# Performance work log

Hardware: AMD Instinct MI355X
Metric: run time of the kernel (lower is better)

The kernel has to match this reference:

```python
import jax, jax.numpy as jnp
import numpy as np

RADIUS = 1.0
NSAMPLE = 1024  # num_votes
EPS = 1e-5     # BatchNorm eps


def _bn2(x, gamma, beta):
    # BatchNorm over [B, C, NS]: stats per channel across (batch, sample)
    m = jnp.mean(x, axis=(0, 2), keepdims=True)
    v = jnp.var(x, axis=(0, 2), keepdims=True)
    return gamma[None, :, None] * (x - m) * jax.lax.rsqrt(v + EPS) + beta[None, :, None]


def _bn1(x, gamma, beta):
    # BatchNorm over [B, C] (conv1d head with length 1): stats across batch
    m = jnp.mean(x, axis=0, keepdims=True)
    v = jnp.var(x, axis=0, keepdims=True)
    return gamma[None, :] * (x - m) * jax.lax.rsqrt(v + EPS) + beta[None, :]


def setup_inputs() -> dict:
    key = jax.random.key(0)
    ks = jax.random.split(key, 16)
    B, N, C = 8, 65536, 256
    def w(k, o, i):
        return jax.random.normal(k, (o, i), jnp.float32) * (1.0 / np.sqrt(i))
    inp = {
        'xyz': jax.random.normal(ks[0], (B, N, 3), jnp.float32),
        'features': jax.random.normal(ks[1], (B, C, N), jnp.float32),
        # shared MLP (conv2d 1x1 + BN + ReLU) x3, input channels = C+3 (use_xyz)
        'w1': w(ks[2], 128, C + 3), 'b1': jnp.zeros(128), 'g1': jnp.ones(128), 'be1': jnp.zeros(128),
        'w2': w(ks[3], 128, 128),   'b2': jnp.zeros(128), 'g2': jnp.ones(128), 'be2': jnp.zeros(128),
        'w3': w(ks[4], 128, 128),   'b3': jnp.zeros(128), 'g3': jnp.ones(128), 'be3': jnp.zeros(128),
        # conv1d head
        'hw1': w(ks[5], 128, 128), 'hb1': jnp.zeros(128), 'hg1': jnp.ones(128), 'hbe1': jnp.zeros(128),
        'hw2': w(ks[6], 128, 128), 'hb2': jnp.zeros(128), 'hg2': jnp.ones(128), 'hbe2': jnp.zeros(128),
        'hw3': w(ks[7], 12, 128),  'hb3': jnp.zeros(12),
    }
    return inp


def reference(xyz, features, w1, b1, g1, be1, w2, b2, g2, be2, w3, b3, g3, be3,
              hw1, hb1, hg1, hbe1, hw2, hb2, hg2, hbe2, hw3, hb3):
    B, N, _ = xyz.shape
    # FPS with npoint=1 deterministically selects point 0
    center = xyz[:, 0, :]                                   # [B,3]
    d2 = jnp.sum((xyz - center[:, None, :]) ** 2, axis=-1)   # [B,N]
    mask = d2 < RADIUS * RADIUS
    ar = jnp.arange(N)
    # ball query: first NSAMPLE in-radius indices (index order), pad with first hit
    order = jnp.argsort(jnp.where(mask, ar, N + ar), axis=1)[:, :NSAMPLE]  # [B,NS]
    valid = jnp.take_along_axis(mask, order, axis=1)
    inds = jnp.where(valid, order, order[:, :1])              # [B,NS]
    g_xyz = (jnp.take_along_axis(xyz, inds[:, :, None], axis=1) - center[:, None, :]) / RADIUS  # [B,NS,3]
    g_feat = jax.vmap(lambda f, i: f[:, i])(features, inds)    # [B,C,NS]
    g = jnp.concatenate([jnp.swapaxes(g_xyz, 1, 2), g_feat], axis=1)  # [B,C+3,NS]

    def mlp(x, w, b, gm, bt):
        y = jnp.einsum('oc,bcn->bon', w, x) + b[None, :, None]
        return jax.nn.relu(_bn2(y, gm, bt))

    h = mlp(g, w1, b1, g1, be1)
    h = mlp(h, w2, b2, g2, be2)
    h = mlp(h, w3, b3, g3, be3)
    f = jnp.max(h, axis=2)                                    # [B,128] maxpool over nsample

    net = jax.nn.relu(_bn1(f @ hw1.T + hb1, hg1, hbe1))
    net = jax.nn.relu(_bn1(net @ hw2.T + hb2, hg2, hbe2))
    net = net @ hw3.T + hb3                                   # [B,12]

    center_out = center + net[:, 0:3]
    size = net[:, 3:6]
    rot_6d = net[:, 6:12]
    return (center_out, size, rot_6d)
```

## Files before the change

kernel.cpp:

```cpp
#include <hip/hip_runtime.h>
#include <hip/hip_bf16.h>
#include <stdint.h>

#define BATCH 8
#define NPTS  65536
#define CFEAT 256
#define K1    259
#define K1PAD 288
#define CH    128
#define NS    1024
#define EPSF  1e-5f
#define INVN  (1.0f / (BATCH * NS))

__device__ __forceinline__ unsigned fenc(float f) {
  unsigned u = __float_as_uint(f);
  return (u & 0x80000000u) ? ~u : (u | 0x80000000u);
}
__device__ __forceinline__ float fdec(unsigned k) {
  unsigned u = (k & 0x80000000u) ? (k & 0x7fffffffu) : ~k;
  return __uint_as_float(u);
}

__global__ __launch_bounds__(1024) void k_select(const float* __restrict__ xyz,
                                                 int* __restrict__ inds,
                                                 float* __restrict__ center,
                                                 float* __restrict__ sums,
                                                 unsigned* __restrict__ maxk,
                                                 unsigned* __restrict__ mink) {
  int b = blockIdx.x;
  int tid = threadIdx.x;
  int lane = tid & 63, wid = tid >> 6;

  if (b == 0) {
    if (tid < 3 * 2 * CH) sums[tid] = 0.f;
    if (tid < BATCH * CH) { maxk[tid] = 0u; mink[tid] = 0xFFFFFFFFu; }
  }

  const float* xb = xyz + (size_t)b * NPTS * 3;
  float cx = xb[0], cy = xb[1], cz = xb[2];
  if (tid < 3) center[b * 3 + tid] = xb[tid];

  __shared__ int wcnt[16];
  int total = 0;
  int* ib = inds + b * NS;

  for (int base = 0; base < NPTS; base += 1024) {
    int i = base + tid;
    float dx = xb[(size_t)i * 3 + 0] - cx;
    float dy = xb[(size_t)i * 3 + 1] - cy;
    float dz = xb[(size_t)i * 3 + 2] - cz;
    float d2 = dx * dx + dy * dy + dz * dz;
    bool pred = d2 < 1.0f;
    unsigned long long bal = __ballot(pred);
    if (lane == 0) wcnt[wid] = (int)__popcll(bal);
    __syncthreads();
    int woff = 0, itot = 0;
#pragma unroll
    for (int w = 0; w < 16; ++w) {
      int c = wcnt[w];
      if (w < wid) woff += c;
      itot += c;
    }
    int pos = total + woff + (int)__popcll(bal & ((1ull << lane) - 1ull));
    if (pred && pos < NS) ib[pos] = i;
    total += itot;
    __syncthreads();
    if (total >= NS) break;
  }
  for (int j = total + tid; j < NS; j += 1024) ib[j] = 0;
}

__device__ __forceinline__ void store_and_stats(float* __restrict__ yb,
                                                float* __restrict__ sums,
                                                const float* __restrict__ bias,
                                                float acc[4][4],
                                                int n0, int tx, int ty) {
#pragma unroll
  for (int r = 0; r < 4; ++r) {
    int o = ty * 4 + r;
    float bs = bias[o];
    float4 v = make_float4(acc[r][0] + bs, acc[r][1] + bs,
                           acc[r][2] + bs, acc[r][3] + bs);
    *(float4*)&yb[(size_t)o * NS + n0 + tx * 4] = v;
    float s = v.x + v.y + v.z + v.w;
    float q = v.x * v.x + v.y * v.y + v.z * v.z + v.w * v.w;
    s += __shfl_xor(s, 1, 64); q += __shfl_xor(q, 1, 64);
    s += __shfl_xor(s, 2, 64); q += __shfl_xor(q, 2, 64);
    s += __shfl_xor(s, 4, 64); q += __shfl_xor(q, 4, 64);
    if (tx == 0) {
      atomicAdd(&sums[o], s);
      atomicAdd(&sums[CH + o], q);
    }
  }
}

__global__ __launch_bounds__(256) void k_gemm1(const float* __restrict__ xyz,
                                               const float* __restrict__ feat,
                                               const int* __restrict__ inds,
                                               const float* __restrict__ center,
                                               const float* __restrict__ W,
                                               const float* __restrict__ bias,
                                               float* __restrict__ y,
                                               float* __restrict__ sums) {
  __shared__ float Ws[32][132];
  __shared__ float Xs[K1PAD][36];
  __shared__ int   ids[32];
  __shared__ float cenl[3];
  int b = blockIdx.y;
  int n0 = blockIdx.x * 32;
  int tid = threadIdx.x;
  if (tid < 32) ids[tid] = inds[b * NS + n0 + tid];
  if (tid < 3)  cenl[tid] = center[b * 3 + tid];
  __syncthreads();

  const float* featb = feat + (size_t)b * CFEAT * NPTS;
  const float* xyzb  = xyz + (size_t)b * NPTS * 3;

  if (tid < 96) {
    int k = tid >> 5, j = tid & 31;
    Xs[k][j] = xyzb[(size_t)ids[j] * 3 + k] - cenl[k];
  }
#pragma unroll 8
  for (int e = tid; e < CFEAT * 32; e += 256) {
    int k = e >> 5, j = e & 31;
    Xs[3 + k][j] = featb[(size_t)k * NPTS + ids[j]];
  }
#pragma unroll
  for (int e = tid; e < 29 * 32; e += 256) {
    Xs[K1 + (e >> 5)][e & 31] = 0.f;
  }

  int tx = tid & 7, ty = tid >> 3;
  float acc[4][4];
#pragma unroll
  for (int r = 0; r < 4; ++r)
#pragma unroll
    for (int j = 0; j < 4; ++j) acc[r][j] = 0.f;

  for (int k0 = 0; k0 < K1PAD; k0 += 32) {
#pragma unroll
    for (int i = 0; i < 16; ++i) {
      int e = tid + 256 * i;
      int o = e >> 5, kk = e & 31;
      int k = k0 + kk;
      Ws[kk][o] = (k < K1) ? W[o * K1 + k] : 0.f;
    }
    __syncthreads();
#pragma unroll
    for (int kk = 0; kk < 32; ++kk) {
      float4 xv = *(const float4*)&Xs[k0 + kk][tx * 4];
      float4 wv = *(const float4*)&Ws[kk][ty * 4];
      acc[0][0] += wv.x * xv.x; acc[0][1] += wv.x * xv.y; acc[0][2] += wv.x * xv.z; acc[0][3] += wv.x * xv.w;
      acc[1][0] += wv.y * xv.x; acc[1][1] += wv.y * xv.y; acc[1][2] += wv.y * xv.z; acc[1][3] += wv.y * xv.w;
      acc[2][0] += wv.z * xv.x; acc[2][1] += wv.z * xv.y; acc[2][2] += wv.z * xv.z; acc[2][3] += wv.z * xv.w;
      acc[3][0] += wv.w * xv.x; acc[3][1] += wv.w * xv.y; acc[3][2] += wv.w * xv.z; acc[3][3] += wv.w * xv.w;
    }
    __syncthreads();
  }
  store_and_stats(y + (size_t)b * CH * NS, sums, bias, acc, n0, tx, ty);
}

template <bool LAST>
__global__ __launch_bounds__(256) void k_gemm23(const float* __restrict__ x,
                                                const float* __restrict__ sums_prev,
                                                const float* __restrict__ gamma,
                                                const float* __restrict__ beta,
                                                const float* __restrict__ W,
                                                const float* __restrict__ bias,
                                                float* __restrict__ y,
                                                float* __restrict__ sums_out,
                                                unsigned* __restrict__ maxk,
                                                unsigned* __restrict__ mink) {
  __shared__ float Ws[32][132];
  __shared__ float Xs[CH][36];
  __shared__ float scl[CH], shf[CH];
  int b = blockIdx.y;
  int n0 = blockIdx.x * 32;
  int tid = threadIdx.x;
  if (tid < CH) {
    float s = sums_prev[tid], q = sums_prev[CH + tid];
    float mean = s * INVN;
    float var = fmaxf(q * INVN - mean * mean, 0.f);
    float sc = gamma[tid] * rsqrtf(var + EPSF);
    scl[tid] = sc;
    shf[tid] = beta[tid] - mean * sc;
  }
  __syncthreads();

  const float* xb = x + (size_t)b * CH * NS;
#pragma unroll
  for (int e = tid; e < CH * 32; e += 256) {
    int k = e >> 5, j = e & 31;
    float v = xb[(size_t)k * NS + n0 + j];
    Xs[k][j] = fmaxf(scl[k] * v + shf[k], 0.f);
  }

  int tx = tid & 7, ty = tid >> 3;
  float acc[4][4];
#pragma unroll
  for (int r = 0; r < 4; ++r)
#pragma unroll
    for (int j = 0; j < 4; ++j) acc[r][j] = 0.f;

  for (int k0 = 0; k0 < CH; k0 += 32) {
#pragma unroll
    for (int i = 0; i < 16; ++i) {
      int e = tid + 256 * i;
      int o = e >> 5, kk = e & 31;
      Ws[kk][o] = W[o * CH + k0 + kk];
    }
    __syncthreads();
#pragma unroll
    for (int kk = 0; kk < 32; ++kk) {
      float4 xv = *(const float4*)&Xs[k0 + kk][tx * 4];
      float4 wv = *(const float4*)&Ws[kk][ty * 4];
      acc[0][0] += wv.x * xv.x; acc[0][1] += wv.x * xv.y; acc[0][2] += wv.x * xv.z; acc[0][3] += wv.x * xv.w;
      acc[1][0] += wv.y * xv.x; acc[1][1] += wv.y * xv.y; acc[1][2] += wv.y * xv.z; acc[1][3] += wv.y * xv.w;
      acc[2][0] += wv.z * xv.x; acc[2][1] += wv.z * xv.y; acc[2][2] += wv.z * xv.z; acc[2][3] += wv.z * xv.w;
      acc[3][0] += wv.w * xv.x; acc[3][1] += wv.w * xv.y; acc[3][2] += wv.w * xv.z; acc[3][3] += wv.w * xv.w;
    }
    __syncthreads();
  }

  if (!LAST) {
    store_and_stats(y + (size_t)b * CH * NS, sums_out, bias, acc, n0, tx, ty);
  } else {
#pragma unroll
    for (int r = 0; r < 4; ++r) {
      int o = ty * 4 + r;
      float bs = bias[o];
      float4 v = make_float4(acc[r][0] + bs, acc[r][1] + bs,
                             acc[r][2] + bs, acc[r][3] + bs);
      float s = v.x + v.y + v.z + v.w;
      float q = v.x * v.x + v.y * v.y + v.z * v.z + v.w * v.w;
      float mx = fmaxf(fmaxf(v.x, v.y), fmaxf(v.z, v.w));
      float mn = fminf(fminf(v.x, v.y), fminf(v.z, v.w));
      s += __shfl_xor(s, 1, 64); q += __shfl_xor(q, 1, 64);
      mx = fmaxf(mx, __shfl_xor(mx, 1, 64)); mn = fminf(mn, __shfl_xor(mn, 1, 64));
      s += __shfl_xor(s, 2, 64); q += __shfl_xor(q, 2, 64);
      mx = fmaxf(mx, __shfl_xor(mx, 2, 64)); mn = fminf(mn, __shfl_xor(mn, 2, 64));
      s += __shfl_xor(s, 4, 64); q += __shfl_xor(q, 4, 64);
      mx = fmaxf(mx, __shfl_xor(mx, 4, 64)); mn = fminf(mn, __shfl_xor(mn, 4, 64));
      if (tx == 0) {
        atomicAdd(&sums_out[o], s);
        atomicAdd(&sums_out[CH + o], q);
        atomicMax(&maxk[b * CH + o], fenc(mx));
        atomicMin(&mink[b * CH + o], fenc(mn));
      }
    }
  }
}

__global__ __launch_bounds__(128) void k_head(const float* __restrict__ sums3,
                                              const float* __restrict__ ga3, const float* __restrict__ be3,
                                              const unsigned* __restrict__ maxk, const unsigned* __restrict__ mink,
                                              const float* __restrict__ hw1, const float* __restrict__ hb1,
                                              const float* __restrict__ hg1, const float* __restrict__ hbe1,
                                              const float* __restrict__ hw2, const float* __restrict__ hb2,
                                              const float* __restrict__ hg2, const float* __restrict__ hbe2,
                                              const float* __restrict__ hw3, const float* __restrict__ hb3,
                                              const float* __restrict__ center,
                                              float* __restrict__ out) {
  __shared__ float A[BATCH * 128];
  __shared__ float Bm[BATCH * 128];
  int c = threadIdx.x;
  {
    float s = sums3[c], q = sums3[CH + c];
    float mean = s * INVN;
    float var = fmaxf(q * INVN - mean * mean, 0.f);
    float sc = ga3[c] * rsqrtf(var + EPSF);
    float sh = be3[c] - mean * sc;
#pragma unroll
    for (int b = 0; b < BATCH; ++b) {
      float ymax = fdec(maxk[b * CH + c]);
      float ymin = fdec(mink[b * CH + c]);
      float ye = (sc >= 0.f) ? ymax : ymin;
      A[b * 128 + c] = fmaxf(sc * ye + sh, 0.f);
    }
  }
  __syncthreads();

  {
    float v[BATCH];
    float bs = hb1[c];
#pragma unroll
    for (int b = 0; b < BATCH; ++b) v[b] = bs;
    const float4* w4 = (const float4*)hw1 + c * 32;
    for (int k4 = 0; k4 < 32; ++k4) {
      float4 w = w4[k4];
#pragma unroll
      for (int b = 0; b < BATCH; ++b) {
        const float* Ar = &A[b * 128 + k4 * 4];
        v[b] += Ar[0] * w.x + Ar[1] * w.y + Ar[2] * w.z + Ar[3] * w.w;
      }
    }
    float m = 0.f;
#pragma unroll
    for (int b = 0; b < BATCH; ++b) m += v[b];
    m *= (1.f / BATCH);
    float var = 0.f;
#pragma unroll
    for (int b = 0; b < BATCH; ++b) { float d = v[b] - m; var += d * d; }
    var *= (1.f / BATCH);
    float r = rsqrtf(var + EPSF);
    float ga = hg1[c], be = hbe1[c];
#pragma unroll
    for (int b = 0; b < BATCH; ++b)
      Bm[b * 128 + c] = fmaxf(ga * (v[b] - m) * r + be, 0.f);
  }
  __syncthreads();

  {
    float v[BATCH];
    float bs = hb2[c];
#pragma unroll
    for (int b = 0; b < BATCH; ++b) v[b] = bs;
    const float4* w4 = (const float4*)hw2 + c * 32;
    for (int k4 = 0; k4 < 32; ++k4) {
      float4 w = w4[k4];
#pragma unroll
      for (int b = 0; b < BATCH; ++b) {
        const float* Br = &Bm[b * 128 + k4 * 4];
        v[b] += Br[0] * w.x + Br[1] * w.y + Br[2] * w.z + Br[3] * w.w;
      }
    }
    float m = 0.f;
#pragma unroll
    for (int b = 0; b < BATCH; ++b) m += v[b];
    m *= (1.f / BATCH);
    float var = 0.f;
#pragma unroll
    for (int b = 0; b < BATCH; ++b) { float d = v[b] - m; var += d * d; }
    var *= (1.f / BATCH);
    float r = rsqrtf(var + EPSF);
    float ga = hg2[c], be = hbe2[c];
#pragma unroll
    for (int b = 0; b < BATCH; ++b)
      A[b * 128 + c] = fmaxf(ga * (v[b] - m) * r + be, 0.f);
  }
  __syncthreads();

  if (c < 96) {
    int b = c / 12, j = c % 12;
    float o = hb3[j];
    const float4* w4 = (const float4*)hw3 + j * 32;
    for (int k4 = 0; k4 < 32; ++k4) {
      float4 w = w4[k4];
      const float* Ar = &A[b * 128 + k4 * 4];
      o += Ar[0] * w.x + Ar[1] * w.y + Ar[2] * w.z + Ar[3] * w.w;
    }
    if (j < 3)      out[b * 3 + j] = center[b * 3 + j] + o;
    else if (j < 6) out[24 + b * 3 + (j - 3)] = o;
    else            out[48 + b * 6 + (j - 6)] = o;
  }
}

extern "C" void kernel_launch(void* const* d_in, const int* in_sizes, int n_in,
                              void* d_out, int out_size, void* d_ws, size_t ws_size,
                              hipStream_t stream) {
  const float* xyz  = (const float*)d_in[0];
  const float* feat = (const float*)d_in[1];
  const float* w1   = (const float*)d_in[2];
  const float* b1   = (const float*)d_in[3];
  const float* ga1  = (const float*)d_in[4];
  const float* be1  = (const float*)d_in[5];
  const float* w2   = (const float*)d_in[6];
  const float* b2   = (const float*)d_in[7];
  const float* ga2  = (const float*)d_in[8];
  const float* be2  = (const float*)d_in[9];
  const float* w3   = (const float*)d_in[10];
  const float* b3   = (const float*)d_in[11];
  const float* ga3  = (const float*)d_in[12];
  const float* be3  = (const float*)d_in[13];
  const float* hw1  = (const float*)d_in[14];
  const float* hb1  = (const float*)d_in[15];
  const float* hg1  = (const float*)d_in[16];
  const float* hbe1 = (const float*)d_in[17];
  const float* hw2  = (const float*)d_in[18];
  const float* hb2  = (const float*)d_in[19];
  const float* hg2  = (const float*)d_in[20];
  const float* hbe2 = (const float*)d_in[21];
  const float* hw3  = (const float*)d_in[22];
  const float* hb3  = (const float*)d_in[23];
  float* out = (float*)d_out;

  char* ws = (char*)d_ws;
  size_t off = 0;
  auto alloc = [&](size_t bytes) -> void* {
    void* p = ws + off;
    off = (off + bytes + 255) & ~(size_t)255;
    return p;
  };
  float*    sums1 = (float*)alloc(2 * CH * 4);
  float*    sums2 = (float*)alloc(2 * CH * 4);
  float*    sums3 = (float*)alloc(2 * CH * 4);
  unsigned* maxk  = (unsigned*)alloc((size_t)BATCH * CH * 4);
  unsigned* mink  = (unsigned*)alloc((size_t)BATCH * CH * 4);
  int*      inds  = (int*)alloc((size_t)BATCH * NS * 4);
  float*    center= (float*)alloc(BATCH * 3 * 4);
  float*    y1    = (float*)alloc((size_t)BATCH * CH * NS * 4);
  float*    y2    = (float*)alloc((size_t)BATCH * CH * NS * 4);

  k_select<<<dim3(BATCH), dim3(1024), 0, stream>>>(xyz, inds, center,
                                                   sums1, maxk, mink);
  k_gemm1<<<dim3(NS / 32, BATCH), dim3(256), 0, stream>>>(xyz, feat, inds, center,
                                                          w1, b1, y1, sums1);
  k_gemm23<false><<<dim3(NS / 32, BATCH), dim3(256), 0, stream>>>(y1, sums1, ga1, be1,
                                                                  w2, b2, y2, sums2,
                                                                  nullptr, nullptr);
  k_gemm23<true><<<dim3(NS / 32, BATCH), dim3(256), 0, stream>>>(y2, sums2, ga2, be2,
                                                                 w3, b3, nullptr, sums3,
                                                                 maxk, mink);
  k_head<<<dim3(1), dim3(128), 0, stream>>>(sums3, ga3, be3, maxk, mink,
                                            hw1, hb1, hg1, hbe1,
                                            hw2, hb2, hg2, hbe2, hw3, hb3,
                                            center, out);
}
```

Measured before the change: 851.4 us.

## Fuse whole pipeline into one cooperative persistent kernel with grid barriers

```diff
diff --git a/kernel.cpp b/kernel.cpp
--- a/kernel.cpp
+++ b/kernel.cpp
@@ -1,5 +1,4 @@
 #include <hip/hip_runtime.h>
-#include <hip/hip_bf16.h>
 #include <stdint.h>
 
 #define BATCH 8
@@ -11,6 +10,8 @@
 #define NS    1024
 #define EPSF  1e-5f
 #define INVN  (1.0f / (BATCH * NS))
+#define WS_STRIDE 132
+#define XS_STRIDE 36
 
 __device__ __forceinline__ unsigned fenc(float f) {
   unsigned u = __float_as_uint(f);
@@ -21,116 +22,199 @@
   return __uint_as_float(u);
 }
 
-__global__ __launch_bounds__(1024) void k_select(const float* __restrict__ xyz,
-                                                 int* __restrict__ inds,
-                                                 float* __restrict__ center,
-                                                 float* __restrict__ sums,
-                                                 unsigned* __restrict__ maxk,
-                                                 unsigned* __restrict__ mink) {
-  int b = blockIdx.x;
-  int tid = threadIdx.x;
-  int lane = tid & 63, wid = tid >> 6;
-
-  if (b == 0) {
-    if (tid < 3 * 2 * CH) sums[tid] = 0.f;
-    if (tid < BATCH * CH) { maxk[tid] = 0u; mink[tid] = 0xFFFFFFFFu; }
-  }
-
-  const float* xb = xyz + (size_t)b * NPTS * 3;
-  float cx = xb[0], cy = xb[1], cz = xb[2];
-  if (tid < 3) center[b * 3 + tid] = xb[tid];
-
-  __shared__ int wcnt[16];
-  int total = 0;
-  int* ib = inds + b * NS;
-
-  for (int base = 0; base < NPTS; base += 1024) {
-    int i = base + tid;
-    float dx = xb[(size_t)i * 3 + 0] - cx;
-    float dy = xb[(size_t)i * 3 + 1] - cy;
-    float dz = xb[(size_t)i * 3 + 2] - cz;
-    float d2 = dx * dx + dy * dy + dz * dz;
-    bool pred = d2 < 1.0f;
-    unsigned long long bal = __ballot(pred);
-    if (lane == 0) wcnt[wid] = (int)__popcll(bal);
-    __syncthreads();
-    int woff = 0, itot = 0;
-#pragma unroll
-    for (int w = 0; w < 16; ++w) {
-      int c = wcnt[w];
-      if (w < wid) woff += c;
-      itot += c;
-    }
-    int pos = total + woff + (int)__popcll(bal & ((1ull << lane) - 1ull));
-    if (pred && pos < NS) ib[pos] = i;
-    total += itot;
-    __syncthreads();
-    if (total >= NS) break;
-  }
-  for (int j = total + tid; j < NS; j += 1024) ib[j] = 0;
-}
-
-__device__ __forceinline__ void store_and_stats(float* __restrict__ yb,
-                                                float* __restrict__ sums,
-                                                const float* __restrict__ bias,
-                                                float acc[4][4],
-                                                int n0, int tx, int ty) {
+__device__ __forceinline__ float aload_f(const float* p) {
+  return __hip_atomic_load(p, __ATOMIC_RELAXED, __HIP_MEMORY_SCOPE_AGENT);
+}
+__device__ __forceinline__ void astore_f(float* p, float v) {
+  __hip_atomic_store(p, v, __ATOMIC_RELAXED, __HIP_MEMORY_SCOPE_AGENT);
+}
+__device__ __forceinline__ int aload_i(const int* p) {
+  return __hip_atomic_load(p, __ATOMIC_RELAXED, __HIP_MEMORY_SCOPE_AGENT);
+}
+__device__ __forceinline__ void astore_i(int* p, int v) {
+  __hip_atomic_store(p, v, __ATOMIC_RELAXED, __HIP_MEMORY_SCOPE_AGENT);
+}
+__device__ __forceinline__ unsigned aload_u(const unsigned* p) {
+  return __hip_atomic_load(p, __ATOMIC_RELAXED, __HIP_MEMORY_SCOPE_AGENT);
+}
+__device__ __forceinline__ void astore_u(unsigned* p, unsigned v) {
+  __hip_atomic_store(p, v, __ATOMIC_RELAXED, __HIP_MEMORY_SCOPE_AGENT);
+}
+
+__device__ __forceinline__ void gsync(unsigned* bar, unsigned target) {
+  __syncthreads();
+  if (threadIdx.x == 0) {
+    __hip_atomic_fetch_add(bar, 1u, __ATOMIC_ACQ_REL, __HIP_MEMORY_SCOPE_AGENT);
+    while (__hip_atomic_load(bar, __ATOMIC_ACQUIRE, __HIP_MEMORY_SCOPE_AGENT) < target)
+      __builtin_amdgcn_s_sleep(2);
+  }
+  __syncthreads();
+}
+
+#define FMA16(wv, xv) do { \
+  acc[0][0] += wv.x*xv.x; acc[0][1] += wv.x*xv.y; acc[0][2] += wv.x*xv.z; acc[0][3] += wv.x*xv.w; \
+  acc[1][0] += wv.y*xv.x; acc[1][1] += wv.y*xv.y; acc[1][2] += wv.y*xv.z; acc[1][3] += wv.y*xv.w; \
+  acc[2][0] += wv.z*xv.x; acc[2][1] += wv.z*xv.y; acc[2][2] += wv.z*xv.z; acc[2][3] += wv.z*xv.w; \
+  acc[3][0] += wv.w*xv.x; acc[3][1] += wv.w*xv.y; acc[3][2] += wv.w*xv.z; acc[3][3] += wv.w*xv.w; \
+} while (0)
+
+struct KParams {
+  const float *xyz, *feat;
+  const float *w1, *b1, *ga1, *be1;
+  const float *w2, *b2, *ga2, *be2;
+  const float *w3, *b3, *ga3, *be3;
+  const float *hw1, *hb1, *hg1, *hbe1;
+  const float *hw2, *hb2, *hg2, *hbe2;
+  const float *hw3, *hb3;
+  int* inds;
+  float* center;
+  float *sums1, *sums2, *sums3;
+  unsigned *maxk, *mink, *bar;
+  float* out;
+};
+
+__device__ __forceinline__ void y_to_lds_and_stats(float* __restrict__ XsB,
+                                                   float* __restrict__ sums,
+                                                   const float* __restrict__ bias,
+                                                   float (&acc)[4][4], int tx, int ty) {
 #pragma unroll
   for (int r = 0; r < 4; ++r) {
     int o = ty * 4 + r;
     float bs = bias[o];
     float4 v = make_float4(acc[r][0] + bs, acc[r][1] + bs,
                            acc[r][2] + bs, acc[r][3] + bs);
-    *(float4*)&yb[(size_t)o * NS + n0 + tx * 4] = v;
+    *(float4*)&XsB[o * XS_STRIDE + tx * 4] = v;
     float s = v.x + v.y + v.z + v.w;
     float q = v.x * v.x + v.y * v.y + v.z * v.z + v.w * v.w;
     s += __shfl_xor(s, 1, 64); q += __shfl_xor(q, 1, 64);
     s += __shfl_xor(s, 2, 64); q += __shfl_xor(q, 2, 64);
     s += __shfl_xor(s, 4, 64); q += __shfl_xor(q, 4, 64);
-    if (tx == 0) {
-      atomicAdd(&sums[o], s);
-      atomicAdd(&sums[CH + o], q);
-    }
-  }
-}
-
-__global__ __launch_bounds__(256) void k_gemm1(const float* __restrict__ xyz,
-                                               const float* __restrict__ feat,
-                                               const int* __restrict__ inds,
-                                               const float* __restrict__ center,
-                                               const float* __restrict__ W,
-                                               const float* __restrict__ bias,
-                                               float* __restrict__ y,
-                                               float* __restrict__ sums) {
-  __shared__ float Ws[32][132];
-  __shared__ float Xs[K1PAD][36];
+    if (tx == 0) { atomicAdd(&sums[o], s); atomicAdd(&sums[CH + o], q); }
+  }
+}
+
+__device__ __forceinline__ void mlp_layer(float* __restrict__ XsB, float* __restrict__ WsB,
+                                          const float* __restrict__ scl_s,
+                                          const float* __restrict__ shf_s,
+                                          const float* __restrict__ W,
+                                          int tid, int tx, int ty, float (&acc)[4][4]) {
+#pragma unroll 16
+  for (int i = 0; i < 64; ++i) {
+    int e = tid + 256 * i;
+    int o = e >> 7, kk = e & 127;
+    WsB[kk * WS_STRIDE + o] = W[o * CH + kk];
+  }
+  __syncthreads();
+#pragma unroll 4
+  for (int i = 0; i < 16; ++i) {
+    int e = tid + 256 * i;
+    int k = e >> 5, j = e & 31;
+    float v = XsB[k * XS_STRIDE + j];
+    XsB[k * XS_STRIDE + j] = fmaxf(scl_s[k] * v + shf_s[k], 0.f);
+  }
+  __syncthreads();
+#pragma unroll 8
+  for (int kk = 0; kk < CH; ++kk) {
+    float4 xv = *(const float4*)&XsB[kk * XS_STRIDE + tx * 4];
+    float4 wv = *(const float4*)&WsB[kk * WS_STRIDE + ty * 4];
+    FMA16(wv, xv);
+  }
+  __syncthreads();
+}
+
+__global__ __launch_bounds__(256, 1) void k_fused(KParams P) {
+  __shared__ float WsBig[CH * WS_STRIDE];
+  __shared__ float Xs[K1PAD * XS_STRIDE];
+  __shared__ float scl[CH], shf[CH];
   __shared__ int   ids[32];
   __shared__ float cenl[3];
-  int b = blockIdx.y;
-  int n0 = blockIdx.x * 32;
+  __shared__ int   wsum[2][4];
+
+  int blk = blockIdx.x;
   int tid = threadIdx.x;
-  if (tid < 32) ids[tid] = inds[b * NS + n0 + tid];
-  if (tid < 3)  cenl[tid] = center[b * 3 + tid];
-  __syncthreads();
-
-  const float* featb = feat + (size_t)b * CFEAT * NPTS;
-  const float* xyzb  = xyz + (size_t)b * NPTS * 3;
-
+
+  if (blk < BATCH) {
+    const float* xb = P.xyz + (size_t)blk * NPTS * 3;
+    if (tid < 3) astore_f(&P.center[blk * 3 + tid], xb[tid]);
+    float cx = xb[0], cy = xb[1], cz = xb[2];
+    int* ib = P.inds + blk * NS;
+    int lane = tid & 63, wid = tid >> 6;
+    int total = 0, par = 0;
+    for (int base = 0; base < NPTS && total < NS; base += 1024) {
+      int i0 = base + tid * 4;
+      const float* pp = &xb[(size_t)i0 * 3];
+      float4 q0 = *(const float4*)pp;
+      float4 q1 = *(const float4*)(pp + 4);
+      float4 q2 = *(const float4*)(pp + 8);
+      float dx, dy, dz;
+      dx = q0.x - cx; dy = q0.y - cy; dz = q0.z - cz; bool p0 = dx*dx + dy*dy + dz*dz < 1.f;
+      dx = q0.w - cx; dy = q1.x - cy; dz = q1.y - cz; bool p1 = dx*dx + dy*dy + dz*dz < 1.f;
+      dx = q1.z - cx; dy = q1.w - cy; dz = q2.x - cz; bool p2 = dx*dx + dy*dy + dz*dz < 1.f;
+      dx = q2.y - cx; dy = q2.z - cy; dz = q2.w - cz; bool p3 = dx*dx + dy*dy + dz*dz < 1.f;
+      int cnt = (int)p0 + (int)p1 + (int)p2 + (int)p3;
+      int scan = cnt;
+#pragma unroll
+      for (int o = 1; o < 64; o <<= 1) {
+        int t = __shfl_up(scan, o, 64);
+        if (lane >= o) scan += t;
+      }
+      if (lane == 63) wsum[par][wid] = scan;
+      __syncthreads();
+      int w0 = wsum[par][0], w1_ = wsum[par][1], w2_ = wsum[par][2], w3_ = wsum[par][3];
+      int woff = (wid > 0 ? w0 : 0) + (wid > 1 ? w1_ : 0) + (wid > 2 ? w2_ : 0);
+      int pos = total + woff + (scan - cnt);
+      if (p0 && pos < NS) astore_i(&ib[pos], i0);     pos += p0;
+      if (p1 && pos < NS) astore_i(&ib[pos], i0 + 1); pos += p1;
+      if (p2 && pos < NS) astore_i(&ib[pos], i0 + 2); pos += p2;
+      if (p3 && pos < NS) astore_i(&ib[pos], i0 + 3); pos += p3;
+      total += w0 + w1_ + w2_ + w3_;
+      par ^= 1;
+    }
+    for (int j = total + tid; j < NS; j += 256) astore_i(&ib[j], 0);
+  } else if (blk == 8) {
+    if (tid < 2 * CH) {
+      astore_f(&P.sums1[tid], 0.f);
+      astore_f(&P.sums2[tid], 0.f);
+      astore_f(&P.sums3[tid], 0.f);
+    }
+#pragma unroll
+    for (int i = 0; i < 4; ++i) {
+      int e = tid + 256 * i;
+      astore_u(&P.maxk[e], 0u);
+      astore_u(&P.mink[e], 0xFFFFFFFFu);
+    }
+  }
+  gsync(P.bar, 256);
+
+  int b = blk >> 5;
+  int n0 = (blk & 31) * 32;
+  int tx = tid & 7, ty = tid >> 3;
+
+  if (tid < 32) ids[tid] = aload_i(&P.inds[b * NS + n0 + tid]);
+  if (tid < 3)  cenl[tid] = aload_f(&P.center[b * 3 + tid]);
+  __syncthreads();
+
+  const float* featb = P.feat + (size_t)b * CFEAT * NPTS;
+  const float* xyzb  = P.xyz + (size_t)b * NPTS * 3;
   if (tid < 96) {
     int k = tid >> 5, j = tid & 31;
-    Xs[k][j] = xyzb[(size_t)ids[j] * 3 + k] - cenl[k];
-  }
-#pragma unroll 8
-  for (int e = tid; e < CFEAT * 32; e += 256) {
-    int k = e >> 5, j = e & 31;
-    Xs[3 + k][j] = featb[(size_t)k * NPTS + ids[j]];
-  }
-#pragma unroll
-  for (int e = tid; e < 29 * 32; e += 256) {
-    Xs[K1 + (e >> 5)][e & 31] = 0.f;
-  }
-
-  int tx = tid & 7, ty = tid >> 3;
+    Xs[k * XS_STRIDE + j] = xyzb[(size_t)ids[j] * 3 + k] - cenl[k];
+  }
+  for (int e = tid; e < 29 * 32; e += 256)
+    Xs[(K1 + (e >> 5)) * XS_STRIDE + (e & 31)] = 0.f;
+  {
+    int j = tid & 31, kbase = tid >> 5;
+    const float* fp = featb + ids[j];
+    float g[32];
+#pragma unroll
+    for (int i = 0; i < 32; ++i)
+      g[i] = fp[(size_t)(kbase + 8 * i) * NPTS];
+#pragma unroll
+    for (int i = 0; i < 32; ++i)
+      Xs[(3 + kbase + 8 * i) * XS_STRIDE + j] = g[i];
+  }
+  __syncthreads();
+
   float acc[4][4];
 #pragma unroll
   for (int r = 0; r < 4; ++r)
@@ -143,247 +227,169 @@
       int e = tid + 256 * i;
       int o = e >> 5, kk = e & 31;
       int k = k0 + kk;
-      Ws[kk][o] = (k < K1) ? W[o * K1 + k] : 0.f;
+      WsBig[kk * WS_STRIDE + o] = (k < K1) ? P.w1[o * K1 + k] : 0.f;
     }
     __syncthreads();
 #pragma unroll
     for (int kk = 0; kk < 32; ++kk) {
-      float4 xv = *(const float4*)&Xs[k0 + kk][tx * 4];
-      float4 wv = *(const float4*)&Ws[kk][ty * 4];
-      acc[0][0] += wv.x * xv.x; acc[0][1] += wv.x * xv.y; acc[0][2] += wv.x * xv.z; acc[0][3] += wv.x * xv.w;
-      acc[1][0] += wv.y * xv.x; acc[1][1] += wv.y * xv.y; acc[1][2] += wv.y * xv.z; acc[1][3] += wv.y * xv.w;
-      acc[2][0] += wv.z * xv.x; acc[2][1] += wv.z * xv.y; acc[2][2] += wv.z * xv.z; acc[2][3] += wv.z * xv.w;
-      acc[3][0] += wv.w * xv.x; acc[3][1] += wv.w * xv.y; acc[3][2] += wv.w * xv.z; acc[3][3] += wv.w * xv.w;
+      float4 xv = *(const float4*)&Xs[(k0 + kk) * XS_STRIDE + tx * 4];
+      float4 wv = *(const float4*)&WsBig[kk * WS_STRIDE + ty * 4];
+      FMA16(wv, xv);
     }
     __syncthreads();
   }
-  store_and_stats(y + (size_t)b * CH * NS, sums, bias, acc, n0, tx, ty);
-}
-
-template <bool LAST>
-__global__ __launch_bounds__(256) void k_gemm23(const float* __restrict__ x,
-                                                const float* __restrict__ sums_prev,
-                                                const float* __restrict__ gamma,
-                                                const float* __restrict__ beta,
-                                                const float* __restrict__ W,
-                                                const float* __restrict__ bias,
-                                                float* __restrict__ y,
-                                                float* __restrict__ sums_out,
-                                                unsigned* __restrict__ maxk,
-                                                unsigned* __restrict__ mink) {
-  __shared__ float Ws[32][132];
-  __shared__ float Xs[CH][36];
-  __shared__ float scl[CH], shf[CH];
-  int b = blockIdx.y;
-  int n0 = blockIdx.x * 32;
-  int tid = threadIdx.x;
+  y_to_lds_and_stats(Xs, P.sums1, P.b1, acc, tx, ty);
+  gsync(P.bar, 512);
+
   if (tid < CH) {
-    float s = sums_prev[tid], q = sums_prev[CH + tid];
+    float s = aload_f(&P.sums1[tid]), q = aload_f(&P.sums1[CH + tid]);
     float mean = s * INVN;
     float var = fmaxf(q * INVN - mean * mean, 0.f);
-    float sc = gamma[tid] * rsqrtf(var + EPSF);
-    scl[tid] = sc;
-    shf[tid] = beta[tid] - mean * sc;
-  }
-  __syncthreads();
-
-  const float* xb = x + (size_t)b * CH * NS;
-#pragma unroll
-  for (int e = tid; e < CH * 32; e += 256) {
-    int k = e >> 5, j = e & 31;
-    float v = xb[(size_t)k * NS + n0 + j];
-    Xs[k][j] = fmaxf(scl[k] * v + shf[k], 0.f);
-  }
-
-  int tx = tid & 7, ty = tid >> 3;
-  float acc[4][4];
+    float sc = P.ga1[tid] * rsqrtf(var + EPSF);
+    scl[tid] = sc; shf[tid] = P.be1[tid] - mean * sc;
+  }
 #pragma unroll
   for (int r = 0; r < 4; ++r)
 #pragma unroll
     for (int j = 0; j < 4; ++j) acc[r][j] = 0.f;
-
-  for (int k0 = 0; k0 < CH; k0 += 32) {
-#pragma unroll
-    for (int i = 0; i < 16; ++i) {
-      int e = tid + 256 * i;
-      int o = e >> 5, kk = e & 31;
-      Ws[kk][o] = W[o * CH + k0 + kk];
-    }
-    __syncthreads();
-#pragma unroll
-    for (int kk = 0; kk < 32; ++kk) {
-      float4 xv = *(const float4*)&Xs[k0 + kk][tx * 4];
-      float4 wv = *(const float4*)&Ws[kk][ty * 4];
-      acc[0][0] += wv.x * xv.x; acc[0][1] += wv.x * xv.y; acc[0][2] += wv.x * xv.z; acc[0][3] += wv.x * xv.w;
-      acc[1][0] += wv.y * xv.x; acc[1][1] += wv.y * xv.y; acc[1][2] += wv.y * xv.z; acc[1][3] += wv.y * xv.w;
-      acc[2][0] += wv.z * xv.x; acc[2][1] += wv.z * xv.y; acc[2][2] += wv.z * xv.z; acc[2][3] += wv.z * xv.w;
-      acc[3][0] += wv.w * xv.x; acc[3][1] += wv.w * xv.y; acc[3][2] += wv.w * xv.z; acc[3][3] += wv.w * xv.w;
-    }
-    __syncthreads();
-  }
-
-  if (!LAST) {
-    store_and_stats(y + (size_t)b * CH * NS, sums_out, bias, acc, n0, tx, ty);
-  } else {
-#pragma unroll
-    for (int r = 0; r < 4; ++r) {
-      int o = ty * 4 + r;
-      float bs = bias[o];
-      float4 v = make_float4(acc[r][0] + bs, acc[r][1] + bs,
-                             acc[r][2] + bs, acc[r][3] + bs);
-      float s = v.x + v.y + v.z + v.w;
-      float q = v.x * v.x + v.y * v.y + v.z * v.z + v.w * v.w;
-      float mx = fmaxf(fmaxf(v.x, v.y), fmaxf(v.z, v.w));
-      float mn = fminf(fminf(v.x, v.y), fminf(v.z, v.w));
-      s += __shfl_xor(s, 1, 64); q += __shfl_xor(q, 1, 64);
-      mx = fmaxf(mx, __shfl_xor(mx, 1, 64)); mn = fminf(mn, __shfl_xor(mn, 1, 64));
-      s += __shfl_xor(s, 2, 64); q += __shfl_xor(q, 2, 64);
-      mx = fmaxf(mx, __shfl_xor(mx, 2, 64)); mn = fminf(mn, __shfl_xor(mn, 2, 64));
-      s += __shfl_xor(s, 4, 64); q += __shfl_xor(q, 4, 64);
-      mx = fmaxf(mx, __shfl_xor(mx, 4, 64)); mn = fminf(mn, __shfl_xor(mn, 4, 64));
-      if (tx == 0) {
-        atomicAdd(&sums_out[o], s);
-        atomicAdd(&sums_out[CH + o], q);
-        atomicMax(&maxk[b * CH + o], fenc(mx));
-        atomicMin(&mink[b * CH + o], fenc(mn));
-      }
-    }
-  }
-}
-
-__global__ __launch_bounds__(128) void k_head(const float* __restrict__ sums3,
-                                              const float* __restrict__ ga3, const float* __restrict__ be3,
-                                              const unsigned* __restrict__ maxk, const unsigned* __restrict__ mink,
-                                              const float* __restrict__ hw1, const float* __restrict__ hb1,
-                                              const float* __restrict__ hg1, const float* __restrict__ hbe1,
-                                              const float* __restrict__ hw2, const float* __restrict__ hb2,
-                                              const float* __restrict__ hg2, const float* __restrict__ hbe2,
-                                              const float* __restrict__ hw3, const float* __restrict__ hb3,
-                                              const float* __restrict__ center,
-                                              float* __restrict__ out) {
-  __shared__ float A[BATCH * 128];
-  __shared__ float Bm[BATCH * 128];
-  int c = threadIdx.x;
-  {
-    float s = sums3[c], q = sums3[CH + c];
+  mlp_layer(Xs, WsBig, scl, shf, P.w2, tid, tx, ty, acc);
+  y_to_lds_and_stats(Xs, P.sums2, P.b2, acc, tx, ty);
+  gsync(P.bar, 768);
+
+  if (tid < CH) {
+    float s = aload_f(&P.sums2[tid]), q = aload_f(&P.sums2[CH + tid]);
     float mean = s * INVN;
     float var = fmaxf(q * INVN - mean * mean, 0.f);
-    float sc = ga3[c] * rsqrtf(var + EPSF);
-    float sh = be3[c] - mean * sc;
-#pragma unroll
-    for (int b = 0; b < BATCH; ++b) {
-      float ymax = fdec(maxk[b * CH + c]);
-      float ymin = fdec(mink[b * CH + c]);
-      float ye = (sc >= 0.f) ? ymax : ymin;
-      A[b * 128 + c] = fmaxf(sc * ye + sh, 0.f);
-    }
-  }
-  __syncthreads();
-
-  {
-    float v[BATCH];
-    float bs = hb1[c];
-#pragma unroll
-    for (int b = 0; b < BATCH; ++b) v[b] = bs;
-    const float4* w4 = (const float4*)hw1 + c * 32;
-    for (int k4 = 0; k4 < 32; ++k4) {
-      float4 w = w4[k4];
-#pragma unroll
-      for (int b = 0; b < BATCH; ++b) {
-        const float* Ar = &A[b * 128 + k4 * 4];
-        v[b] += Ar[0] * w.x + Ar[1] * w.y + Ar[2] * w.z + Ar[3] * w.w;
+    float sc = P.ga2[tid] * rsqrtf(var + EPSF);
+    scl[tid] = sc; shf[tid] = P.be2[tid] - mean * sc;
+  }
+#pragma unroll
+  for (int r = 0; r < 4; ++r)
+#pragma unroll
+    for (int j = 0; j < 4; ++j) acc[r][j] = 0.f;
+  mlp_layer(Xs, WsBig, scl, shf, P.w3, tid, tx, ty, acc);
+
+#pragma unroll
+  for (int r = 0; r < 4; ++r) {
+    int o = ty * 4 + r;
+    float bs = P.b3[o];
+    float4 v = make_float4(acc[r][0] + bs, acc[r][1] + bs,
+                           acc[r][2] + bs, acc[r][3] + bs);
+    float s = v.x + v.y + v.z + v.w;
+    float q = v.x * v.x + v.y * v.y + v.z * v.z + v.w * v.w;
+    float mx = fmaxf(fmaxf(v.x, v.y), fmaxf(v.z, v.w));
+    float mn = fminf(fminf(v.x, v.y), fminf(v.z, v.w));
+    s += __shfl_xor(s, 1, 64); q += __shfl_xor(q, 1, 64);
+    mx = fmaxf(mx, __shfl_xor(mx, 1, 64)); mn = fminf(mn, __shfl_xor(mn, 1, 64));
+    s += __shfl_xor(s, 2, 64); q += __shfl_xor(q, 2, 64);
+    mx = fmaxf(mx, __shfl_xor(mx, 2, 64)); mn = fminf(mn, __shfl_xor(mn, 2, 64));
+    s += __shfl_xor(s, 4, 64); q += __shfl_xor(q, 4, 64);
+    mx = fmaxf(mx, __shfl_xor(mx, 4, 64)); mn = fminf(mn, __shfl_xor(mn, 4, 64));
+    if (tx == 0) {
+      atomicAdd(&P.sums3[o], s);
+      atomicAdd(&P.sums3[CH + o], q);
+      atomicMax(&P.maxk[b * CH + o], fenc(mx));
+      atomicMin(&P.mink[b * CH + o], fenc(mn));
+    }
+  }
+  gsync(P.bar, 1024);
+
+  if (blk == 0) {
+    float* A  = Xs;
+    float* Bm = Xs + 1024;
+    int c = tid;
+    if (c < CH) {
+      float s = aload_f(&P.sums3[c]), q = aload_f(&P.sums3[CH + c]);
+      float mean = s * INVN;
+      float var = fmaxf(q * INVN - mean * mean, 0.f);
+      float sc = P.ga3[c] * rsqrtf(var + EPSF);
+      float sh = P.be3[c] - mean * sc;
+#pragma unroll
+      for (int bb = 0; bb < BATCH; ++bb) {
+        float ymax = fdec(aload_u(&P.maxk[bb * CH + c]));
+        float ymin = fdec(aload_u(&P.mink[bb * CH + c]));
+        float ye = (sc >= 0.f) ? ymax : ymin;
+        A[bb * CH + c] = fmaxf(sc * ye + sh, 0.f);
       }
     }
-    float m = 0.f;
-#pragma unroll
-    for (int b = 0; b < BATCH; ++b) m += v[b];
-    m *= (1.f / BATCH);
-    float var = 0.f;
-#pragma unroll
-    for (int b = 0; b < BATCH; ++b) { float d = v[b] - m; var += d * d; }
-    var *= (1.f / BATCH);
-    float r = rsqrtf(var + EPSF);
-    float ga = hg1[c], be = hbe1[c];
-#pragma unroll
-    for (int b = 0; b < BATCH; ++b)
-      Bm[b * 128 + c] = fmaxf(ga * (v[b] - m) * r + be, 0.f);
-  }
-  __syncthreads();
-
-  {
-    float v[BATCH];
-    float bs = hb2[c];
-#pragma unroll
-    for (int b = 0; b < BATCH; ++b) v[b] = bs;
-    const float4* w4 = (const float4*)hw2 + c * 32;
-    for (int k4 = 0; k4 < 32; ++k4) {
-      float4 w = w4[k4];
-#pragma unroll
-      for (int b = 0; b < BATCH; ++b) {
-        const float* Br = &Bm[b * 128 + k4 * 4];
-        v[b] += Br[0] * w.x + Br[1] * w.y + Br[2] * w.z + Br[3] * w.w;
+    __syncthreads();
+    if (c < CH) {
+      float v[BATCH];
+      float bs = P.hb1[c];
+#pragma unroll
+      for (int bb = 0; bb < BATCH; ++bb) v[bb] = bs;
+      const float4* w4 = (const float4*)P.hw1 + c * 32;
+      for (int k4 = 0; k4 < 32; ++k4) {
+        float4 w = w4[k4];
+#pragma unroll
+        for (int bb = 0; bb < BATCH; ++bb) {
+          const float* Ar = &A[bb * CH + k4 * 4];
+          v[bb] += Ar[0] * w.x + Ar[1] * w.y + Ar[2] * w.z + Ar[3] * w.w;
+        }
       }
-    }
-    float m = 0.f;
-#pragma unroll
-    for (int b = 0; b < BATCH; ++b) m += v[b];
-    m *= (1.f / BATCH);
-    float var = 0.f;
-#pragma unroll
-    for (int b = 0; b < BATCH; ++b) { float d = v[b] - m; var += d * d; }
-    var *= (1.f / BATCH);
-    float r = rsqrtf(var + EPSF);
-    float ga = hg2[c], be = hbe2[c];
-#pragma unroll
-    for (int b = 0; b < BATCH; ++b)
-      A[b * 128 + c] = fmaxf(ga * (v[b] - m) * r + be, 0.f);
-  }
-  __syncthreads();
-
-  if (c < 96) {
-    int b = c / 12, j = c % 12;
-    float o = hb3[j];
-    const float4* w4 = (const float4*)hw3 + j * 32;
-    for (int k4 = 0; k4 < 32; ++k4) {
-      float4 w = w4[k4];
-      const float* Ar = &A[b * 128 + k4 * 4];
-      o += Ar[0] * w.x + Ar[1] * w.y + Ar[2] * w.z + Ar[3] * w.w;
-    }
-    if (j < 3)      out[b * 3 + j] = center[b * 3 + j] + o;
-    else if (j < 6) out[24 + b * 3 + (j - 3)] = o;
-    else            out[48 + b * 6 + (j - 6)] = o;
+      float m = 0.f;
+#pragma unroll
+      for (int bb = 0; bb < BATCH; ++bb) m += v[bb];
+      m *= (1.f / BATCH);
+      float var = 0.f;
+#pragma unroll
+      for (int bb = 0; bb < BATCH; ++bb) { float d = v[bb] - m; var += d * d; }
+      var *= (1.f / BATCH);
+      float r = rsqrtf(var + EPSF);
+      float ga = P.hg1[c], be = P.hbe1[c];
+#pragma unroll
+      for (int bb = 0; bb < BATCH; ++bb)
+        Bm[bb * CH + c] = fmaxf(ga * (v[bb] - m) * r + be, 0.f);
+    }
+    __syncthreads();
+    if (c < CH) {
+      float v[BATCH];
+      float bs = P.hb2[c];
+#pragma unroll
+      for (int bb = 0; bb < BATCH; ++bb) v[bb] = bs;
+      const float4* w4 = (const float4*)P.hw2 + c * 32;
+      for (int k4 = 0; k4 < 32; ++k4) {
+        float4 w = w4[k4];
+#pragma unroll
+        for (int bb = 0; bb < BATCH; ++bb) {
+          const float* Br = &Bm[bb * CH + k4 * 4];
+          v[bb] += Br[0] * w.x + Br[1] * w.y + Br[2] * w.z + Br[3] * w.w;
+        }
+      }
+      float m = 0.f;
+#pragma unroll
+      for (int bb = 0; bb < BATCH; ++bb) m += v[bb];
+      m *= (1.f / BATCH);
+      float var = 0.f;
+#pragma unroll
+      for (int bb = 0; bb < BATCH; ++bb) { float d = v[bb] - m; var += d * d; }
+      var *= (1.f / BATCH);
+      float r = rsqrtf(var + EPSF);
+      float ga = P.hg2[c], be = P.hbe2[c];
+#pragma unroll
+      for (int bb = 0; bb < BATCH; ++bb)
+        A[bb * CH + c] = fmaxf(ga * (v[bb] - m) * r + be, 0.f);
+    }
+    __syncthreads();
+    if (c < 96) {
+      int bb = c / 12, j = c % 12;
+      float o = P.hb3[j];
+      const float4* w4 = (const float4*)P.hw3 + j * 32;
+      for (int k4 = 0; k4 < 32; ++k4) {
+        float4 w = w4[k4];
+        const float* Ar = &A[bb * CH + k4 * 4];
+        o += Ar[0] * w.x + Ar[1] * w.y + Ar[2] * w.z + Ar[3] * w.w;
+      }
+      if (j < 3)      P.out[bb * 3 + j] = aload_f(&P.center[bb * 3 + j]) + o;
+      else if (j < 6) P.out[24 + bb * 3 + (j - 3)] = o;
+      else            P.out[48 + bb * 6 + (j - 6)] = o;
+    }
   }
 }
 
 extern "C" void kernel_launch(void* const* d_in, const int* in_sizes, int n_in,
                               void* d_out, int out_size, void* d_ws, size_t ws_size,
                               hipStream_t stream) {
-  const float* xyz  = (const float*)d_in[0];
-  const float* feat = (const float*)d_in[1];
-  const float* w1   = (const float*)d_in[2];
-  const float* b1   = (const float*)d_in[3];
-  const float* ga1  = (const float*)d_in[4];
-  const float* be1  = (const float*)d_in[5];
-  const float* w2   = (const float*)d_in[6];
-  const float* b2   = (const float*)d_in[7];
-  const float* ga2  = (const float*)d_in[8];
-  const float* be2  = (const float*)d_in[9];
-  const float* w3   = (const float*)d_in[10];
-  const float* b3   = (const float*)d_in[11];
-  const float* ga3  = (const float*)d_in[12];
-  const float* be3  = (const float*)d_in[13];
-  const float* hw1  = (const float*)d_in[14];
-  const float* hb1  = (const float*)d_in[15];
-  const float* hg1  = (const float*)d_in[16];
-  const float* hbe1 = (const float*)d_in[17];
-  const float* hw2  = (const float*)d_in[18];
-  const float* hb2  = (const float*)d_in[19];
-  const float* hg2  = (const float*)d_in[20];
-  const float* hbe2 = (const float*)d_in[21];
-  const float* hw3  = (const float*)d_in[22];
-  const float* hb3  = (const float*)d_in[23];
-  float* out = (float*)d_out;
-
   char* ws = (char*)d_ws;
   size_t off = 0;
   auto alloc = [&](size_t bytes) -> void* {
@@ -391,28 +397,48 @@
     off = (off + bytes + 255) & ~(size_t)255;
     return p;
   };
-  float*    sums1 = (float*)alloc(2 * CH * 4);
-  float*    sums2 = (float*)alloc(2 * CH * 4);
-  float*    sums3 = (float*)alloc(2 * CH * 4);
-  unsigned* maxk  = (unsigned*)alloc((size_t)BATCH * CH * 4);
-  unsigned* mink  = (unsigned*)alloc((size_t)BATCH * CH * 4);
-  int*      inds  = (int*)alloc((size_t)BATCH * NS * 4);
-  float*    center= (float*)alloc(BATCH * 3 * 4);
-  float*    y1    = (float*)alloc((size_t)BATCH * CH * NS * 4);
-  float*    y2    = (float*)alloc((size_t)BATCH * CH * NS * 4);
-
-  k_select<<<dim3(BATCH), dim3(1024), 0, stream>>>(xyz, inds, center,
-                                                   sums1, maxk, mink);
-  k_gemm1<<<dim3(NS / 32, BATCH), dim3(256), 0, stream>>>(xyz, feat, inds, center,
-                                                          w1, b1, y1, sums1);
-  k_gemm23<false><<<dim3(NS / 32, BATCH), dim3(256), 0, stream>>>(y1, sums1, ga1, be1,
-                                                                  w2, b2, y2, sums2,
-                                                                  nullptr, nullptr);
-  k_gemm23<true><<<dim3(NS / 32, BATCH), dim3(256), 0, stream>>>(y2, sums2, ga2, be2,
-                                                                 w3, b3, nullptr, sums3,
-                                                                 maxk, mink);
-  k_head<<<dim3(1), dim3(128), 0, stream>>>(sums3, ga3, be3, maxk, mink,
-                                            hw1, hb1, hg1, hbe1,
-                                            hw2, hb2, hg2, hbe2, hw3, hb3,
-                                            center, out);
-}
+  float*    sums1  = (float*)alloc(2 * CH * 4);
+  float*    sums2  = (float*)alloc(2 * CH * 4);
+  float*    sums3  = (float*)alloc(2 * CH * 4);
+  unsigned* maxk   = (unsigned*)alloc((size_t)BATCH * CH * 4);
+  unsigned* mink   = (unsigned*)alloc((size_t)BATCH * CH * 4);
+  int*      inds   = (int*)alloc((size_t)BATCH * NS * 4);
+  float*    center = (float*)alloc(BATCH * 3 * 4);
+  unsigned* bar    = (unsigned*)alloc(256);
+
+  KParams P;
+  P.xyz  = (const float*)d_in[0];
+  P.feat = (const float*)d_in[1];
+  P.w1   = (const float*)d_in[2];
+  P.b1   = (const float*)d_in[3];
+  P.ga1  = (const float*)d_in[4];
+  P.be1  = (const float*)d_in[5];
+  P.w2   = (const float*)d_in[6];
+  P.b2   = (const float*)d_in[7];
+  P.ga2  = (const float*)d_in[8];
+  P.be2  = (const float*)d_in[9];
+  P.w3   = (const float*)d_in[10];
+  P.b3   = (const float*)d_in[11];
+  P.ga3  = (const float*)d_in[12];
+  P.be3  = (const float*)d_in[13];
+  P.hw1  = (const float*)d_in[14];
+  P.hb1  = (const float*)d_in[15];
+  P.hg1  = (const float*)d_in[16];
+  P.hbe1 = (const float*)d_in[17];
+  P.hw2  = (const float*)d_in[18];
+  P.hb2  = (const float*)d_in[19];
+  P.hg2  = (const float*)d_in[20];
+  P.hbe2 = (const float*)d_in[21];
+  P.hw3  = (const float*)d_in[22];
+  P.hb3  = (const float*)d_in[23];
+  P.inds = inds; P.center = center;
+  P.sums1 = sums1; P.sums2 = sums2; P.sums3 = sums3;
+  P.maxk = maxk; P.mink = mink; P.bar = bar;
+  P.out = (float*)d_out;
+
+  hipMemsetAsync(bar, 0, 4, stream);
+
+  void* args[] = { &P };
+  hipLaunchCooperativeKernel(reinterpret_cast<const void*>(&k_fused),
+                             dim3(256), dim3(256), args, 0, stream);
+}
```

Measured after the change: 980.6 us. 15.2% more time.
